# Performance work log

Measured on AMD Instinct MI355X. Metric: run time of the kernel, lower is better.

## Reference

```python
import jax, jax.numpy as jnp
import numpy as np

B, C, H, W = 2, 512, 48, 48
HEADS = 8          # head_dim = C // HEADS = 64
GROUPS = 32        # min(32, ceil(512/4)) = 32
EPS = 1e-5


def setup_inputs() -> dict:
    key = jax.random.key(0)
    ks = jax.random.split(key, 5)
    return {
        "x": jax.random.normal(ks[0], (B, C, H, W), jnp.float32),
        "gn_w": jnp.ones((C,), jnp.float32),
        "gn_b": jnp.zeros((C,), jnp.float32),
        # 1x1 convs stored as [out, in] matrices
        "qkv_w": jax.random.normal(ks[1], (3 * C, C), jnp.float32) / np.float32(np.sqrt(C)),
        "qkv_b": jax.random.normal(ks[2], (3 * C,), jnp.float32) * 0.01,
        "proj_w": jax.random.normal(ks[3], (C, C), jnp.float32) / np.float32(np.sqrt(C)),
        "proj_b": jax.random.normal(ks[4], (C,), jnp.float32) * 0.01,
    }


def _group_norm(x, w, b):
    b_, c_, h_, w_ = x.shape
    xg = x.reshape(b_, GROUPS, c_ // GROUPS, h_, w_)
    mean = xg.mean(axis=(2, 3, 4), keepdims=True)
    var = xg.var(axis=(2, 3, 4), keepdims=True)  # biased, matches F.group_norm
    xn = ((xg - mean) * jax.lax.rsqrt(var + EPS)).reshape(b_, c_, h_, w_)
    return xn * w[None, :, None, None] + b[None, :, None, None]


def reference(x, gn_w, gn_b, qkv_w, qkv_b, proj_w, proj_b):
    bx, cx, hx, wx = x.shape
    d = cx // HEADS
    n = hx * wx
    xn = _group_norm(x, gn_w, gn_b)
    # qkv 1x1 conv -> [B, 3C, H, W]
    y = jnp.einsum('oc,bchw->bohw', qkv_w, xn) + qkv_b[None, :, None, None]
    # torch: y.reshape(B*heads, d, 3, N).unbind(2)  (channel layout: head, chan, qkv)
    qkv = y.reshape(bx * HEADS, d, 3, n)
    q, k, v = qkv[:, :, 0, :], qkv[:, :, 1, :], qkv[:, :, 2, :]
    scale = np.float32(1.0 / np.sqrt(d))
    # AttentionOp: fp32 QK^T + softmax over keys (axis=2)
    w_attn = jax.nn.softmax(jnp.einsum('ncq,nck->nqk', q, k * scale), axis=2)
    a = jnp.einsum('nqk,nck->ncq', w_attn, v).reshape(bx, cx, hx, wx)
    out = jnp.einsum('oc,bchw->bohw', proj_w, a) + proj_b[None, :, None, None]
    return out + x
```

## Files before the change

kernel.cpp:

```cpp
#include <hip/hip_runtime.h>

typedef __bf16 bf16;
typedef __bf16 bf16x8 __attribute__((ext_vector_type(8)));
typedef __bf16 bf16x4 __attribute__((ext_vector_type(4)));
typedef float f32x4 __attribute__((ext_vector_type(4)));

#define B_ 2
#define C_ 512
#define HW_ 2304
#define GROUPS_ 32
#define CPG_ 16
#define EPS_ 1e-5f
#define THR_ 8.0f
#define LOG2E_ 1.44269504f
#define EXP2(x) __builtin_amdgcn_exp2f(x)

__device__ __forceinline__ void gload_lds16(const bf16* g, bf16* l) {
  __builtin_amdgcn_global_load_lds((const __attribute__((address_space(1))) void*)g,
                                   (__attribute__((address_space(3))) void*)l, 16, 0, 0);
}

__global__ __launch_bounds__(256) void pre_k(const float* __restrict__ x,
                                             const float* __restrict__ qkv_w,
                                             const float* __restrict__ qkv_b,
                                             const float* __restrict__ proj_w,
                                             float* __restrict__ ps,
                                             float* __restrict__ pss,
                                             bf16* __restrict__ wqkv,
                                             bf16* __restrict__ wp,
                                             float* __restrict__ bqkv) {
  int blk = blockIdx.x;
  if (blk < 512) {
    int bg = blk >> 3, seg = blk & 7;
    const int n4 = CPG_ * HW_ / 4 / 8;
    const float4* p = (const float4*)(x + (long)bg * CPG_ * HW_) + (long)seg * n4;
    float s = 0.f, ss = 0.f;
    for (int i = threadIdx.x; i < n4; i += 256) {
      float4 v = p[i];
      s += v.x + v.y + v.z + v.w;
      ss += v.x * v.x + v.y * v.y + v.z * v.z + v.w * v.w;
    }
#pragma unroll
    for (int d = 1; d < 64; d <<= 1) { s += __shfl_xor(s, d); ss += __shfl_xor(ss, d); }
    __shared__ float rs[4], rss[4];
    int wave = threadIdx.x >> 6, lane = threadIdx.x & 63;
    if (lane == 0) { rs[wave] = s; rss[wave] = ss; }
    __syncthreads();
    if (threadIdx.x == 0) {
      ps[blk] = rs[0] + rs[1] + rs[2] + rs[3];
      pss[blk] = rss[0] + rss[1] + rss[2] + rss[3];
    }
  } else {
    int idx = (blk - 512) * 256 + threadIdx.x;
    int r = idx >> 9, c = idx & 511;
    int src = (r < 512) ? 3 * r : (r < 1024 ? 3 * (r - 512) + 1 : 3 * (r - 1024) + 2);
    float sc = (r < 512) ? 0.125f * LOG2E_ : 1.0f;
    wqkv[idx] = (bf16)(qkv_w[(long)src * 512 + c] * sc);
    if (idx < 512 * 512) wp[idx] = (bf16)(proj_w[idx]);
    if (idx < 1536) {
      int sb = (idx < 512) ? 3 * idx : (idx < 1024 ? 3 * (idx - 512) + 1 : 3 * (idx - 1024) + 2);
      float sc2 = (idx < 512) ? 0.125f * LOG2E_ : 1.0f;
      bqkv[idx] = qkv_b[sb] * sc2;
    }
  }
}

__global__ __launch_bounds__(256) void gn_apply_k(const float* __restrict__ x,
                                                  const float* __restrict__ gw,
                                                  const float* __restrict__ gb,
                                                  const float* __restrict__ ps,
                                                  const float* __restrict__ pss,
                                                  bf16* __restrict__ xnT) {
  int n0 = blockIdx.x * 64, c0 = blockIdx.y * 32, b = blockIdx.z;
  int nn = n0 + (threadIdx.x & 63);
  int cb = c0 + ((threadIdx.x >> 6) << 3);
  __shared__ float smu[2], srstd[2];
  if (threadIdx.x < 2) {
    int gi = b * GROUPS_ + (c0 >> 4) + threadIdx.x;
    float s = 0.f, ss = 0.f;
#pragma unroll
    for (int k = 0; k < 8; ++k) { s += ps[gi * 8 + k]; ss += pss[gi * 8 + k]; }
    const float invN = 1.0f / (float)(CPG_ * HW_);
    float mu = s * invN;
    float var = ss * invN - mu * mu;
    smu[threadIdx.x] = mu;
    srstd[threadIdx.x] = rsqrtf(var + EPS_);
  }
  __syncthreads();
  int gsel = threadIdx.x >> 7;
  float mu = smu[gsel], rstd = srstd[gsel];
  bf16x8 o;
#pragma unroll
  for (int j = 0; j < 8; ++j) {
    int c = cb + j;
    float sc = rstd * gw[c];
    float sh = gb[c] - mu * sc;
    float v = x[((long)b * C_ + c) * HW_ + nn];
    o[j] = (bf16)(v * sc + sh);
  }
  *(bf16x8*)&xnT[((long)b * HW_ + nn) * C_ + cb] = o;
}

__global__ __launch_bounds__(512) void gemm_qkv_k(const bf16* __restrict__ A,
                                                  const bf16* __restrict__ BT,
                                                  const float* __restrict__ bias,
                                                  bf16* __restrict__ yT,
                                                  bf16* __restrict__ vOut) {
  constexpr int KK = 512;
  constexpr int NSTEP = KK >> 6;
  int b = blockIdx.z;
  A += (long)HW_ * 512 * b;
  yT += (long)HW_ * 1024 * b;
  vOut += (long)512 * HW_ * b;
  int m0 = blockIdx.y * 128, n0 = blockIdx.x * 64;
  int tid = threadIdx.x, lane = tid & 63, wave = tid >> 6;
  int wm = (wave >> 1) << 5, wn = (wave & 1) << 5;
  int fr = lane & 15, g = lane >> 4;
  __shared__ __align__(16) bf16 As[3][128 * 64];
  __shared__ __align__(16) bf16 Bs[3][64 * 64];
  int sr = tid >> 3;
  int swz = (((tid & 7) + sr) & 7) << 3;
  const bf16* gA = A + (long)(m0 + sr) * KK + swz;
  const bf16* gA2 = A + (long)(m0 + 64 + sr) * KK + swz;
  const bf16* gB = BT + (long)(n0 + sr) * KK + swz;
  int o0 = ((g - fr) & 7) << 3;
  int o1 = ((4 + g - fr) & 7) << 3;
  f32x4 acc[2][2] = {};
  gload_lds16(gA, &As[0][tid * 8]);
  gload_lds16(gA2, &As[0][4096 + tid * 8]);
  gload_lds16(gB, &Bs[0][tid * 8]);
  gload_lds16(gA + 64, &As[1][tid * 8]);
  gload_lds16(gA2 + 64, &As[1][4096 + tid * 8]);
  gload_lds16(gB + 64, &Bs[1][tid * 8]);
  asm volatile("s_waitcnt vmcnt(3)" ::: "memory");
  __builtin_amdgcn_s_barrier();
#pragma unroll
  for (int t = 0; t < NSTEP; ++t) {
    const int cur = t % 3;
    if (t + 2 < NSTEP) {
      const int nb = (t + 2) % 3;
      int k0 = (t + 2) << 6;
      gload_lds16(gA + k0, &As[nb][tid * 8]);
      gload_lds16(gA2 + k0, &As[nb][4096 + tid * 8]);
      gload_lds16(gB + k0, &Bs[nb][tid * 8]);
    }
    bf16x8 a00 = *(bf16x8*)&As[cur][(wm + fr) * 64 + o0];
    bf16x8 a01 = *(bf16x8*)&As[cur][(wm + fr) * 64 + o1];
    bf16x8 a10 = *(bf16x8*)&As[cur][(wm + 16 + fr) * 64 + o0];
    bf16x8 a11 = *(bf16x8*)&As[cur][(wm + 16 + fr) * 64 + o1];
    bf16x8 b00 = *(bf16x8*)&Bs[cur][(wn + fr) * 64 + o0];
    bf16x8 b01 = *(bf16x8*)&Bs[cur][(wn + fr) * 64 + o1];
    bf16x8 b10 = *(bf16x8*)&Bs[cur][(wn + 16 + fr) * 64 + o0];
    bf16x8 b11 = *(bf16x8*)&Bs[cur][(wn + 16 + fr) * 64 + o1];
    acc[0][0] = __builtin_amdgcn_mfma_f32_16x16x32_bf16(a00, b00, acc[0][0], 0, 0, 0);
    acc[0][0] = __builtin_amdgcn_mfma_f32_16x16x32_bf16(a01, b01, acc[0][0], 0, 0, 0);
    acc[0][1] = __builtin_amdgcn_mfma_f32_16x16x32_bf16(a00, b10, acc[0][1], 0, 0, 0);
    acc[0][1] = __builtin_amdgcn_mfma_f32_16x16x32_bf16(a01, b11, acc[0][1], 0, 0, 0);
    acc[1][0] = __builtin_amdgcn_mfma_f32_16x16x32_bf16(a10, b00, acc[1][0], 0, 0, 0);
    acc[1][0] = __builtin_amdgcn_mfma_f32_16x16x32_bf16(a11, b01, acc[1][0], 0, 0, 0);
    acc[1][1] = __builtin_amdgcn_mfma_f32_16x16x32_bf16(a10, b10, acc[1][1], 0, 0, 0);
    acc[1][1] = __builtin_amdgcn_mfma_f32_16x16x32_bf16(a11, b11, acc[1][1], 0, 0, 0);
    if (t + 2 < NSTEP) {
      asm volatile("s_waitcnt vmcnt(3) lgkmcnt(0)" ::: "memory");
    } else if (t + 1 < NSTEP) {
      asm volatile("s_waitcnt vmcnt(0) lgkmcnt(0)" ::: "memory");
    }
    if (t + 1 < NSTEP) __builtin_amdgcn_s_barrier();
  }
  int rbase = (lane >> 4) << 2;
  if (n0 < 1024) {
#pragma unroll
    for (int mi = 0; mi < 2; ++mi)
#pragma unroll
      for (int nj = 0; nj < 2; ++nj)
#pragma unroll
        for (int reg = 0; reg < 4; ++reg) {
          int row = m0 + wm + (mi << 4) + rbase + reg;
          int col = n0 + wn + (nj << 4) + fr;
          yT[(long)row * 1024 + col] = (bf16)(acc[mi][nj][reg] + bias[col]);
        }
  } else {
#pragma unroll
    for (int mi = 0; mi < 2; ++mi)
#pragma unroll
      for (int nj = 0; nj < 2; ++nj) {
        int row0 = m0 + wm + (mi << 4) + rbase;
        int ch = n0 - 1024 + wn + (nj << 4) + fr;
        float bs = bias[n0 + wn + (nj << 4) + fr];
        bf16x4 ov = {(bf16)(acc[mi][nj][0] + bs), (bf16)(acc[mi][nj][1] + bs),
                     (bf16)(acc[mi][nj][2] + bs), (bf16)(acc[mi][nj][3] + bs)};
        *(bf16x4*)&vOut[(long)ch * HW_ + row0] = ov;
      }
  }
}

__global__ __launch_bounds__(512) void gemm_proj_k(const bf16* __restrict__ A,
                                                   const bf16* __restrict__ BT,
                                                   const float* __restrict__ bias,
                                                   const float* __restrict__ resid,
                                                   float* __restrict__ Cc) {
  constexpr int KK = 512;
  constexpr int NSTEP = KK >> 6;
  int b = blockIdx.z;
  BT += (long)HW_ * 512 * b;
  const float* R = resid + (long)512 * HW_ * b;
  Cc += (long)512 * HW_ * b;
  int m0 = blockIdx.y * 128, n0 = blockIdx.x * 64;
  int tid = threadIdx.x, lane = tid & 63, wave = tid >> 6;
  int wm = (wave >> 1) << 5, wn = (wave & 1) << 5;
  int fr = lane & 15, g = lane >> 4;
  __shared__ __align__(16) bf16 As[3][128 * 64];
  __shared__ __align__(16) bf16 Bs[3][64 * 64];
  int sr = tid >> 3;
  int swz = (((tid & 7) + sr) & 7) << 3;
  const bf16* gA = A + (long)(m0 + sr) * KK + swz;
  const bf16* gA2 = A + (long)(m0 + 64 + sr) * KK + swz;
  const bf16* gB = BT + (long)(n0 + sr) * KK + swz;
  int o0 = ((g - fr) & 7) << 3;
  int o1 = ((4 + g - fr) & 7) << 3;
  f32x4 acc[2][2] = {};
  gload_lds16(gA, &As[0][tid * 8]);
  gload_lds16(gA2, &As[0][4096 + tid * 8]);
  gload_lds16(gB, &Bs[0][tid * 8]);
  gload_lds16(gA + 64, &As[1][tid * 8]);
  gload_lds16(gA2 + 64, &As[1][4096 + tid * 8]);
  gload_lds16(gB + 64, &Bs[1][tid * 8]);
  asm volatile("s_waitcnt vmcnt(3)" ::: "memory");
  __builtin_amdgcn_s_barrier();
#pragma unroll
  for (int t = 0; t < NSTEP; ++t) {
    const int cur = t % 3;
    if (t + 2 < NSTEP) {
      const int nb = (t + 2) % 3;
      int k0 = (t + 2) << 6;
      gload_lds16(gA + k0, &As[nb][tid * 8]);
      gload_lds16(gA2 + k0, &As[nb][4096 + tid * 8]);
      gload_lds16(gB + k0, &Bs[nb][tid * 8]);
    }
    bf16x8 a00 = *(bf16x8*)&As[cur][(wm + fr) * 64 + o0];
    bf16x8 a01 = *(bf16x8*)&As[cur][(wm + fr) * 64 + o1];
    bf16x8 a10 = *(bf16x8*)&As[cur][(wm + 16 + fr) * 64 + o0];
    bf16x8 a11 = *(bf16x8*)&As[cur][(wm + 16 + fr) * 64 + o1];
    bf16x8 b00 = *(bf16x8*)&Bs[cur][(wn + fr) * 64 + o0];
    bf16x8 b01 = *(bf16x8*)&Bs[cur][(wn + fr) * 64 + o1];
    bf16x8 b10 = *(bf16x8*)&Bs[cur][(wn + 16 + fr) * 64 + o0];
    bf16x8 b11 = *(bf16x8*)&Bs[cur][(wn + 16 + fr) * 64 + o1];
    acc[0][0] = __builtin_amdgcn_mfma_f32_16x16x32_bf16(a00, b00, acc[0][0], 0, 0, 0);
    acc[0][0] = __builtin_amdgcn_mfma_f32_16x16x32_bf16(a01, b01, acc[0][0], 0, 0, 0);
    acc[0][1] = __builtin_amdgcn_mfma_f32_16x16x32_bf16(a00, b10, acc[0][1], 0, 0, 0);
    acc[0][1] = __builtin_amdgcn_mfma_f32_16x16x32_bf16(a01, b11, acc[0][1], 0, 0, 0);
    acc[1][0] = __builtin_amdgcn_mfma_f32_16x16x32_bf16(a10, b00, acc[1][0], 0, 0, 0);
    acc[1][0] = __builtin_amdgcn_mfma_f32_16x16x32_bf16(a11, b01, acc[1][0], 0, 0, 0);
    acc[1][1] = __builtin_amdgcn_mfma_f32_16x16x32_bf16(a10, b10, acc[1][1], 0, 0, 0);
    acc[1][1] = __builtin_amdgcn_mfma_f32_16x16x32_bf16(a11, b11, acc[1][1], 0, 0, 0);
    if (t + 2 < NSTEP) {
      asm volatile("s_waitcnt vmcnt(3) lgkmcnt(0)" ::: "memory");
    } else if (t + 1 < NSTEP) {
      asm volatile("s_waitcnt vmcnt(0) lgkmcnt(0)" ::: "memory");
    }
    if (t + 1 < NSTEP) __builtin_amdgcn_s_barrier();
  }
  int rbase = (lane >> 4) << 2;
#pragma unroll
  for (int mi = 0; mi < 2; ++mi)
#pragma unroll
    for (int nj = 0; nj < 2; ++nj)
#pragma unroll
      for (int reg = 0; reg < 4; ++reg) {
        int row = m0 + wm + (mi << 4) + rbase + reg;
        int col = n0 + wn + (nj << 4) + fr;
        Cc[(long)row * HW_ + col] =
            acc[mi][nj][reg] + bias[row] + R[(long)row * HW_ + col];
      }
}

template <int NS>
__global__ __launch_bounds__(512) void attn_k(const bf16* __restrict__ yT,
                                              const bf16* __restrict__ V,
                                              bf16* __restrict__ Op,
                                              float* __restrict__ Mp,
                                              float* __restrict__ Lp) {
  const int n = HW_;
  constexpr int NT = (HW_ / NS) / 64;
  int bh = blockIdx.y, b = bh >> 3, h = bh & 7;
  int split = blockIdx.z;
  int q0 = blockIdx.x * 128;
  int kbeg = split * (n / NS);
  int tid = threadIdx.x, lane = tid & 63, wave = tid >> 6;
  int fr = lane & 15, g = lane >> 4, kg = g << 3;
  const bf16* yTb = yT + (long)b * n * 1024;
  const bf16* Vb = V + ((long)b * C_ + h * 64) * n;
  const bf16* Kb = yTb + 512 + h * 64;

  int qrow = q0 + (wave << 4) + fr;
  const bf16* qp = yTb + (long)qrow * 1024 + h * 64;
  bf16x8 qf0 = *(const bf16x8*)(qp + kg);
  bf16x8 qf1 = *(const bf16x8*)(qp + 32 + kg);

  __shared__ __align__(16) bf16 Kt[2][64][64];
  __shared__ __align__(16) bf16 Vt[2][64][64];

  int o0 = ((g + fr) & 7) << 3;
  int o1 = ((4 + g + fr) & 7) << 3;

  float m_run = -1e30f, l_run = 0.f;
  f32x4 oacc[4] = {};

  int r0 = tid >> 3;
  int ck = tid & 7;
  int c0e = ck << 3;
  int pk = ((ck + r0) & 7) << 3;
  int vs = (c0e & 32) | ((c0e & 8) << 1) | ((c0e & 16) >> 2);
  int cv = vs >> 3, sub = vs & 7;
  int pv0 = (((cv + r0) & 7) << 3) + sub;
  int pv1 = (((cv + 1 + r0) & 7) << 3) + sub;

  const bf16* kptr = Kb + (long)(kbeg + r0) * 1024 + c0e;
  const bf16* vptr = Vb + (long)r0 * n + kbeg + c0e;
  uint4 rk = *(const uint4*)kptr;
  uint4 rv = *(const uint4*)vptr;
  *(uint4*)&Kt[0][r0][pk] = rk;
  *(uint2*)&Vt[0][r0][pv0] = make_uint2(rv.x, rv.y);
  *(uint2*)&Vt[0][r0][pv1] = make_uint2(rv.z, rv.w);
  kptr += 64 * 1024;
  vptr += 64;
  rk = *(const uint4*)kptr;
  rv = *(const uint4*)vptr;
  __syncthreads();

  for (int t = 0; t < NT; ++t) {
    int cur = t & 1;
    f32x4 s[4] = {};
    __builtin_amdgcn_s_setprio(1);
#pragma unroll
    for (int nj = 0; nj < 4; ++nj) {
      bf16x8 kf0 = *(bf16x8*)&Kt[cur][(nj << 4) + fr][o0];
      bf16x8 kf1 = *(bf16x8*)&Kt[cur][(nj << 4) + fr][o1];
      s[nj] = __builtin_amdgcn_mfma_f32_16x16x32_bf16(kf0, qf0, s[nj], 0, 0, 0);
      s[nj] = __builtin_amdgcn_mfma_f32_16x16x32_bf16(kf1, qf1, s[nj], 0, 0, 0);
    }
    __builtin_amdgcn_s_setprio(0);
    if (t + 1 < NT) {
      int nb = cur ^ 1;
      *(uint4*)&Kt[nb][r0][pk] = rk;
      *(uint2*)&Vt[nb][r0][pv0] = make_uint2(rv.x, rv.y);
      *(uint2*)&Vt[nb][r0][pv1] = make_uint2(rv.z, rv.w);
      if (t + 2 < NT) {
        kptr += 64 * 1024;
        vptr += 64;
        rk = *(const uint4*)kptr;
        rv = *(const uint4*)vptr;
      }
    }
    float pm = fmaxf(fmaxf(s[0][0], s[0][1]), fmaxf(s[0][2], s[0][3]));
#pragma unroll
    for (int nj = 1; nj < 4; ++nj)
      pm = fmaxf(pm, fmaxf(fmaxf(s[nj][0], s[nj][1]), fmaxf(s[nj][2], s[nj][3])));
    pm = fmaxf(pm, __shfl_xor(pm, 16));
    pm = fmaxf(pm, __shfl_xor(pm, 32));
    if (__any(pm > m_run + THR_)) {
      float mn = fmaxf(m_run, pm);
      float corr = EXP2(m_run - mn);
      m_run = mn;
      l_run *= corr;
#pragma unroll
      for (int dj = 0; dj < 4; ++dj)
#pragma unroll
        for (int r = 0; r < 4; ++r) oacc[dj][r] *= corr;
    }
    float ls = 0.f;
    bf16x8 pa0, pa1;
#pragma unroll
    for (int r = 0; r < 4; ++r) {
      float p0 = EXP2(s[0][r] - m_run);
      float p1 = EXP2(s[1][r] - m_run);
      float p2 = EXP2(s[2][r] - m_run);
      float p3 = EXP2(s[3][r] - m_run);
      ls += (p0 + p1) + (p2 + p3);
      pa0[r] = (bf16)p0;
      pa0[4 + r] = (bf16)p1;
      pa1[r] = (bf16)p2;
      pa1[4 + r] = (bf16)p3;
    }
    ls += __shfl_xor(ls, 16);
    ls += __shfl_xor(ls, 32);
    l_run += ls;
    __builtin_amdgcn_s_setprio(1);
#pragma unroll
    for (int dj = 0; dj < 4; ++dj) {
      bf16x8 vf0 = *(bf16x8*)&Vt[cur][(dj << 4) + fr][o0];
      bf16x8 vf1 = *(bf16x8*)&Vt[cur][(dj << 4) + fr][o1];
      oacc[dj] = __builtin_amdgcn_mfma_f32_16x16x32_bf16(vf0, pa0, oacc[dj], 0, 0, 0);
      oacc[dj] = __builtin_amdgcn_mfma_f32_16x16x32_bf16(vf1, pa1, oacc[dj], 0, 0, 0);
    }
    __builtin_amdgcn_s_setprio(0);
    __syncthreads();
  }
  long orow = (long)(split * 16 + bh) * n + q0 + (wave << 4) + fr;
#pragma unroll
  for (int dj = 0; dj < 4; ++dj) {
    bf16x4 ov = {(bf16)oacc[dj][0], (bf16)oacc[dj][1], (bf16)oacc[dj][2], (bf16)oacc[dj][3]};
    *(bf16x4*)&Op[orow * 64 + (dj << 4) + (g << 2)] = ov;
  }
  if (g == 0) {
    Mp[orow] = m_run;
    Lp[orow] = l_run;
  }
}

template <int NS>
__global__ __launch_bounds__(256) void attn_merge_k(const bf16* __restrict__ Op,
                                                    const float* __restrict__ Mp,
                                                    const float* __restrict__ Lp,
                                                    bf16* __restrict__ aT) {
  int bh = blockIdx.y, b = bh >> 3, h = bh & 7;
  int gi = blockIdx.x * 256 + threadIdx.x;
  int nrow = gi >> 3, dd8 = (gi & 7) << 3;
  long idx[NS];
  float mm = -1e30f;
#pragma unroll
  for (int s = 0; s < NS; ++s) {
    idx[s] = (long)(s * 16 + bh) * HW_ + nrow;
    mm = fmaxf(mm, Mp[idx[s]]);
  }
  float l = 0.f, w[NS];
#pragma unroll
  for (int s = 0; s < NS; ++s) {
    w[s] = EXP2(Mp[idx[s]] - mm);
    l += Lp[idx[s]] * w[s];
  }
  float invl = 1.f / l;
  float oaccf[8] = {};
#pragma unroll
  for (int s = 0; s < NS; ++s) {
    bf16x8 o = *(const bf16x8*)&Op[idx[s] * 64 + dd8];
    float ws = w[s] * invl;
#pragma unroll
    for (int j = 0; j < 8; ++j) oaccf[j] += (float)o[j] * ws;
  }
  bf16x8 o;
#pragma unroll
  for (int j = 0; j < 8; ++j) o[j] = (bf16)oaccf[j];
  *(bf16x8*)&aT[((long)b * HW_ + nrow) * C_ + h * 64 + dd8] = o;
}

extern "C" void kernel_launch(void* const* d_in, const int* in_sizes, int n_in,
                              void* d_out, int out_size, void* d_ws, size_t ws_size,
                              hipStream_t stream) {
  const float* x = (const float*)d_in[0];
  const float* gn_w = (const float*)d_in[1];
  const float* gn_b = (const float*)d_in[2];
  const float* qkv_w = (const float*)d_in[3];
  const float* qkv_b = (const float*)d_in[4];
  const float* proj_w = (const float*)d_in[5];
  const float* proj_b = (const float*)d_in[6];
  float* out = (float*)d_out;

  char* ws = (char*)d_ws;
  float* ps = (float*)ws;    ws += 2048;
  float* pss = (float*)ws;   ws += 2048;
  float* bqkv = (float*)ws;  ws += 6144;
  bf16* wqkv = (bf16*)ws;    ws += 1536l * 512 * 2;
  bf16* wp = (bf16*)ws;      ws += 512l * 512 * 2;
  bf16* xnT = (bf16*)ws;     ws += 2l * HW_ * 512 * 2;
  bf16* yT = (bf16*)ws;      ws += 2l * HW_ * 1024 * 2;
  bf16* v = (bf16*)ws;       ws += 2l * 512 * HW_ * 2;
  bf16* aT = (bf16*)ws;      ws += 2l * HW_ * 512 * 2;
  bf16* Op = (bf16*)ws;
  size_t base_used = (size_t)(ws - (char*)d_ws);
  size_t need4 = base_used + 4ull * 16 * HW_ * 64 * 2 + 2ull * 4 * 16 * HW_ * 4;
  int NS = (ws_size >= need4) ? 4 : 2;
  ws += (size_t)NS * 16 * HW_ * 64 * 2;
  float* Mp = (float*)ws;    ws += (size_t)NS * 16 * HW_ * 4;
  float* Lp = (float*)ws;    ws += (size_t)NS * 16 * HW_ * 4;

  pre_k<<<3584, 256, 0, stream>>>(x, qkv_w, qkv_b, proj_w, ps, pss, wqkv, wp, bqkv);
  gn_apply_k<<<dim3(36, 16, 2), 256, 0, stream>>>(x, gn_w, gn_b, ps, pss, xnT);
  gemm_qkv_k<<<dim3(24, 18, 2), 512, 0, stream>>>(xnT, wqkv, bqkv, yT, v);
  if (NS == 4) {
    attn_k<4><<<dim3(18, 16, 4), 512, 0, stream>>>(yT, v, Op, Mp, Lp);
    attn_merge_k<4><<<dim3(72, 16), 256, 0, stream>>>(Op, Mp, Lp, aT);
  } else {
    attn_k<2><<<dim3(18, 16, 2), 512, 0, stream>>>(yT, v, Op, Mp, Lp);
    attn_merge_k<2><<<dim3(72, 16), 256, 0, stream>>>(Op, Mp, Lp, aT);
  }
  gemm_proj_k<<<dim3(36, 4, 2), 512, 0, stream>>>(wp, aT, proj_b, x, out);
}
```

Measured before the change: 84.73 us.

## Process attention key tiles in pairs with four-stage LDS ring buffer

The attention kernel now handles two 64-key tiles per iteration. It uses a 4-deep shared-memory ring for K/V, issues two register prefetches ahead, and does one online-softmax max/rescale per pair. This halves the number of barriers and softmax correction steps and gives the compiler more independent MFMA work to interleave. In exchange LDS use doubles to 64KB per block and register pressure rises, which may lower occupancy. Odd tile counts are handled by a tail step.

```diff
diff --git a/kernel.cpp b/kernel.cpp
--- a/kernel.cpp
+++ b/kernel.cpp
@@ -282,6 +282,8 @@
                                               float* __restrict__ Lp) {
   const int n = HW_;
   constexpr int NT = (HW_ / NS) / 64;
+  constexpr int NPAIR = NT / 2;
+  constexpr int TAIL = NT & 1;
   int bh = blockIdx.y, b = bh >> 3, h = bh & 7;
   int split = blockIdx.z;
   int q0 = blockIdx.x * 128;
@@ -297,8 +299,8 @@
   bf16x8 qf0 = *(const bf16x8*)(qp + kg);
   bf16x8 qf1 = *(const bf16x8*)(qp + 32 + kg);
 
-  __shared__ __align__(16) bf16 Kt[2][64][64];
-  __shared__ __align__(16) bf16 Vt[2][64][64];
+  __shared__ __align__(16) bf16 Kt[4][64][64];
+  __shared__ __align__(16) bf16 Vt[4][64][64];
 
   int o0 = ((g + fr) & 7) << 3;
   int o1 = ((4 + g + fr) & 7) << 3;
@@ -315,43 +317,122 @@
   int pv0 = (((cv + r0) & 7) << 3) + sub;
   int pv1 = (((cv + 1 + r0) & 7) << 3) + sub;
 
-  const bf16* kptr = Kb + (long)(kbeg + r0) * 1024 + c0e;
-  const bf16* vptr = Vb + (long)r0 * n + kbeg + c0e;
-  uint4 rk = *(const uint4*)kptr;
-  uint4 rv = *(const uint4*)vptr;
-  *(uint4*)&Kt[0][r0][pk] = rk;
-  *(uint2*)&Vt[0][r0][pv0] = make_uint2(rv.x, rv.y);
-  *(uint2*)&Vt[0][r0][pv1] = make_uint2(rv.z, rv.w);
-  kptr += 64 * 1024;
-  vptr += 64;
-  rk = *(const uint4*)kptr;
-  rv = *(const uint4*)vptr;
+  const bf16* kbase = Kb + (long)(kbeg + r0) * 1024 + c0e;
+  const bf16* vbase = Vb + (long)r0 * n + kbeg + c0e;
+
+#define LDK_(t) (*(const uint4*)(kbase + (long)(t) * 64 * 1024))
+#define LDV_(t) (*(const uint4*)(vbase + (t) * 64))
+#define WRT_(t, rk, rv)                                          \
+  {                                                              \
+    *(uint4*)&Kt[(t) & 3][r0][pk] = (rk);                        \
+    *(uint2*)&Vt[(t) & 3][r0][pv0] = make_uint2((rv).x, (rv).y); \
+    *(uint2*)&Vt[(t) & 3][r0][pv1] = make_uint2((rv).z, (rv).w); \
+  }
+
+  uint4 rkA = LDK_(0), rvA = LDV_(0);
+  uint4 rkB = LDK_(1), rvB = LDV_(1);
+  WRT_(0, rkA, rvA);
+  WRT_(1, rkB, rvB);
+  if (2 < NT) { rkA = LDK_(2); rvA = LDV_(2); }
+  if (3 < NT) { rkB = LDK_(3); rvB = LDV_(3); }
   __syncthreads();
 
-  for (int t = 0; t < NT; ++t) {
-    int cur = t & 1;
+#pragma unroll
+  for (int p = 0; p < NPAIR; ++p) {
+    const int tA = 2 * p, tB = tA + 1;
+    const int bA = tA & 3, bB = tB & 3;
+    f32x4 sA[4] = {}, sB[4] = {};
+    __builtin_amdgcn_s_setprio(1);
+#pragma unroll
+    for (int nj = 0; nj < 4; ++nj) {
+      bf16x8 kf0 = *(bf16x8*)&Kt[bA][(nj << 4) + fr][o0];
+      bf16x8 kf1 = *(bf16x8*)&Kt[bA][(nj << 4) + fr][o1];
+      sA[nj] = __builtin_amdgcn_mfma_f32_16x16x32_bf16(kf0, qf0, sA[nj], 0, 0, 0);
+      sA[nj] = __builtin_amdgcn_mfma_f32_16x16x32_bf16(kf1, qf1, sA[nj], 0, 0, 0);
+    }
+#pragma unroll
+    for (int nj = 0; nj < 4; ++nj) {
+      bf16x8 kf0 = *(bf16x8*)&Kt[bB][(nj << 4) + fr][o0];
+      bf16x8 kf1 = *(bf16x8*)&Kt[bB][(nj << 4) + fr][o1];
+      sB[nj] = __builtin_amdgcn_mfma_f32_16x16x32_bf16(kf0, qf0, sB[nj], 0, 0, 0);
+      sB[nj] = __builtin_amdgcn_mfma_f32_16x16x32_bf16(kf1, qf1, sB[nj], 0, 0, 0);
+    }
+    __builtin_amdgcn_s_setprio(0);
+    if (tA + 2 < NT) WRT_(tA + 2, rkA, rvA);
+    if (tB + 2 < NT) WRT_(tB + 2, rkB, rvB);
+    if (tA + 4 < NT) { rkA = LDK_(tA + 4); rvA = LDV_(tA + 4); }
+    if (tB + 4 < NT) { rkB = LDK_(tB + 4); rvB = LDV_(tB + 4); }
+    float pm = fmaxf(fmaxf(sA[0][0], sA[0][1]), fmaxf(sA[0][2], sA[0][3]));
+#pragma unroll
+    for (int nj = 1; nj < 4; ++nj)
+      pm = fmaxf(pm, fmaxf(fmaxf(sA[nj][0], sA[nj][1]), fmaxf(sA[nj][2], sA[nj][3])));
+#pragma unroll
+    for (int nj = 0; nj < 4; ++nj)
+      pm = fmaxf(pm, fmaxf(fmaxf(sB[nj][0], sB[nj][1]), fmaxf(sB[nj][2], sB[nj][3])));
+    pm = fmaxf(pm, __shfl_xor(pm, 16));
+    pm = fmaxf(pm, __shfl_xor(pm, 32));
+    if (__any(pm > m_run + THR_)) {
+      float mn = fmaxf(m_run, pm);
+      float corr = EXP2(m_run - mn);
+      m_run = mn;
+      l_run *= corr;
+#pragma unroll
+      for (int dj = 0; dj < 4; ++dj)
+#pragma unroll
+        for (int r = 0; r < 4; ++r) oacc[dj][r] *= corr;
+    }
+    float ls = 0.f;
+    bf16x8 paA0, paA1, paB0, paB1;
+#pragma unroll
+    for (int r = 0; r < 4; ++r) {
+      float a0 = EXP2(sA[0][r] - m_run);
+      float a1 = EXP2(sA[1][r] - m_run);
+      float a2 = EXP2(sA[2][r] - m_run);
+      float a3 = EXP2(sA[3][r] - m_run);
+      float b0 = EXP2(sB[0][r] - m_run);
+      float b1 = EXP2(sB[1][r] - m_run);
+      float b2 = EXP2(sB[2][r] - m_run);
+      float b3 = EXP2(sB[3][r] - m_run);
+      ls += ((a0 + a1) + (a2 + a3)) + ((b0 + b1) + (b2 + b3));
+      paA0[r] = (bf16)a0;
+      paA0[4 + r] = (bf16)a1;
+      paA1[r] = (bf16)a2;
+      paA1[4 + r] = (bf16)a3;
+      paB0[r] = (bf16)b0;
+      paB0[4 + r] = (bf16)b1;
+      paB1[r] = (bf16)b2;
+      paB1[4 + r] = (bf16)b3;
+    }
+    ls += __shfl_xor(ls, 16);
+    ls += __shfl_xor(ls, 32);
+    l_run += ls;
+    __builtin_amdgcn_s_setprio(1);
+#pragma unroll
+    for (int dj = 0; dj < 4; ++dj) {
+      bf16x8 vfA0 = *(bf16x8*)&Vt[bA][(dj << 4) + fr][o0];
+      bf16x8 vfA1 = *(bf16x8*)&Vt[bA][(dj << 4) + fr][o1];
+      oacc[dj] = __builtin_amdgcn_mfma_f32_16x16x32_bf16(vfA0, paA0, oacc[dj], 0, 0, 0);
+      oacc[dj] = __builtin_amdgcn_mfma_f32_16x16x32_bf16(vfA1, paA1, oacc[dj], 0, 0, 0);
+      bf16x8 vfB0 = *(bf16x8*)&Vt[bB][(dj << 4) + fr][o0];
+      bf16x8 vfB1 = *(bf16x8*)&Vt[bB][(dj << 4) + fr][o1];
+      oacc[dj] = __builtin_amdgcn_mfma_f32_16x16x32_bf16(vfB0, paB0, oacc[dj], 0, 0, 0);
+      oacc[dj] = __builtin_amdgcn_mfma_f32_16x16x32_bf16(vfB1, paB1, oacc[dj], 0, 0, 0);
+    }
+    __builtin_amdgcn_s_setprio(0);
+    __syncthreads();
+  }
+  if (TAIL) {
+    constexpr int bT = (NT - 1) & 3;
     f32x4 s[4] = {};
     __builtin_amdgcn_s_setprio(1);
 #pragma unroll
     for (int nj = 0; nj < 4; ++nj) {
-      bf16x8 kf0 = *(bf16x8*)&Kt[cur][(nj << 4) + fr][o0];
-      bf16x8 kf1 = *(bf16x8*)&Kt[cur][(nj << 4) + fr][o1];
+      bf16x8 kf0 = *(bf16x8*)&Kt[bT][(nj << 4) + fr][o0];
+      bf16x8 kf1 = *(bf16x8*)&Kt[bT][(nj << 4) + fr][o1];
       s[nj] = __builtin_amdgcn_mfma_f32_16x16x32_bf16(kf0, qf0, s[nj], 0, 0, 0);
       s[nj] = __builtin_amdgcn_mfma_f32_16x16x32_bf16(kf1, qf1, s[nj], 0, 0, 0);
     }
     __builtin_amdgcn_s_setprio(0);
-    if (t + 1 < NT) {
-      int nb = cur ^ 1;
-      *(uint4*)&Kt[nb][r0][pk] = rk;
-      *(uint2*)&Vt[nb][r0][pv0] = make_uint2(rv.x, rv.y);
-      *(uint2*)&Vt[nb][r0][pv1] = make_uint2(rv.z, rv.w);
-      if (t + 2 < NT) {
-        kptr += 64 * 1024;
-        vptr += 64;
-        rk = *(const uint4*)kptr;
-        rv = *(const uint4*)vptr;
-      }
-    }
     float pm = fmaxf(fmaxf(s[0][0], s[0][1]), fmaxf(s[0][2], s[0][3]));
 #pragma unroll
     for (int nj = 1; nj < 4; ++nj)
@@ -388,14 +469,16 @@
     __builtin_amdgcn_s_setprio(1);
 #pragma unroll
     for (int dj = 0; dj < 4; ++dj) {
-      bf16x8 vf0 = *(bf16x8*)&Vt[cur][(dj << 4) + fr][o0];
-      bf16x8 vf1 = *(bf16x8*)&Vt[cur][(dj << 4) + fr][o1];
+      bf16x8 vf0 = *(bf16x8*)&Vt[bT][(dj << 4) + fr][o0];
+      bf16x8 vf1 = *(bf16x8*)&Vt[bT][(dj << 4) + fr][o1];
       oacc[dj] = __builtin_amdgcn_mfma_f32_16x16x32_bf16(vf0, pa0, oacc[dj], 0, 0, 0);
       oacc[dj] = __builtin_amdgcn_mfma_f32_16x16x32_bf16(vf1, pa1, oacc[dj], 0, 0, 0);
     }
     __builtin_amdgcn_s_setprio(0);
-    __syncthreads();
-  }
+  }
+#undef LDK_
+#undef LDV_
+#undef WRT_
   long orow = (long)(split * 16 + bh) * n + q0 + (wave << 4) + fr;
 #pragma unroll
   for (int dj = 0; dj < 4; ++dj) {
```

New measurement: 83.78 us. Within noise of the previous version (-1.1%).
